# Performance work log

Hardware: AMD Instinct MI355X
Metric: run time of the kernel (lower is better)

The kernel has to match this reference:

```python
import jax, jax.numpy as jnp
import numpy as np

DIM = 64
B, H, W = 4, 80, 80


def setup_inputs() -> dict:
    key = jax.random.key(0)
    k1, k2, k3 = jax.random.split(key, 3)
    x = jax.random.normal(k1, (B, DIM, H, W), dtype=jnp.float32)
    # 1x1 conv == per-pixel linear: weight [3*dim, dim], bias [3*dim]
    w_qkv = jax.random.normal(k2, (3 * DIM, DIM), dtype=jnp.float32) * (1.0 / np.sqrt(DIM).astype(np.float32))
    b_qkv = jax.random.normal(k3, (3 * DIM,), dtype=jnp.float32) * 0.01
    return {"x": x, "w_qkv": w_qkv, "b_qkv": b_qkv}


def reference(x, w_qkv, b_qkv):
    Bb, C, Hh, Ww = x.shape
    N = Hh * Ww
    # 1x1 conv -> qkv, chunked along channels
    qkv = jnp.einsum('bchw,oc->bohw', x, w_qkv) + b_qkv[None, :, None, None]
    q, k, v = jnp.split(qkv, 3, axis=1)  # each [B,C,H,W]

    # --- spatial attention (uses q on both sides, as in the original) ---
    # qk: transpose(3,1) -> [B,W,H,C] -> [B, W*H, C]
    qk = jnp.transpose(q, (0, 3, 2, 1)).reshape(Bb, N, C)
    # kq: [B, C, H*W]  (note: different flatten order than qk, faithful to source)
    kq = q.reshape(Bb, C, N)
    ms = jax.nn.softmax(jnp.matmul(qk, kq), axis=-1)  # [B, N, N]

    # --- channel attention ---
    kf = k.reshape(Bb, C, N)                                # [B, C, N]
    qf = jnp.transpose(q, (0, 3, 2, 1)).reshape(Bb, N, C)   # [B, N, C]
    ma = jax.nn.softmax(jnp.matmul(kf, qf), axis=-1)        # [B, C, C]

    # --- apply to v ---
    vq = jnp.transpose(v, (0, 3, 2, 1)).reshape(Bb, N, C)   # [B, N, C]
    ms_out = jnp.matmul(ms, vq)                             # [B, N, C]
    ms_out = jnp.swapaxes(ms_out, 1, 2).reshape(Bb, C, Hh, Ww)
    ma_out = jnp.matmul(ma, v.reshape(Bb, C, N)).reshape(Bb, C, Hh, Ww)
    return ms_out + ma_out
```

## Files before the change

### kernel.cpp

```cpp
#include <hip/hip_runtime.h>
#include <stdint.h>

#define BATCH 4
#define CH 64
#define HW 80
#define NPIX 6400
#define SPLITS 3

typedef __attribute__((ext_vector_type(8))) short bf16x8;
typedef __attribute__((ext_vector_type(4))) float f32x4;

#define QSCALE 1.2011224087864498f
#define ESHIFT 115.41560327111707f

static __device__ __forceinline__ unsigned short f2bf(float f) {
  union { float f; unsigned int u; } v; v.f = f;
  unsigned int u = v.u;
  return (unsigned short)((u + 0x7fffu + ((u >> 16) & 1u)) >> 16);
}
static __device__ __forceinline__ float bf2f(unsigned short h) {
  union { unsigned int u; float f; } v; v.u = ((unsigned int)h) << 16;
  return v.f;
}
static __device__ __forceinline__ unsigned int split_pack(float a) {
  unsigned short hi = f2bf(a);
  union { unsigned int u; float f; } hf; hf.u = ((unsigned int)hi) << 16;
  unsigned short lo = f2bf(a - hf.f);
  return (unsigned int)hi | ((unsigned int)lo << 16);
}
static __device__ __forceinline__ void deint(uint4 a, uint4 b, bf16x8* h, bf16x8* l) {
  union { unsigned int u[4]; bf16x8 v; } H, L;
  H.u[0] = __builtin_amdgcn_perm(a.y, a.x, 0x05040100u);
  H.u[1] = __builtin_amdgcn_perm(a.w, a.z, 0x05040100u);
  H.u[2] = __builtin_amdgcn_perm(b.y, b.x, 0x05040100u);
  H.u[3] = __builtin_amdgcn_perm(b.w, b.z, 0x05040100u);
  L.u[0] = __builtin_amdgcn_perm(a.y, a.x, 0x07060302u);
  L.u[1] = __builtin_amdgcn_perm(a.w, a.z, 0x07060302u);
  L.u[2] = __builtin_amdgcn_perm(b.y, b.x, 0x07060302u);
  L.u[3] = __builtin_amdgcn_perm(b.w, b.z, 0x07060302u);
  *h = H.v; *l = L.v;
}

__global__ __launch_bounds__(512) void qkv_kernel(
    const float* __restrict__ x, const float* __restrict__ w,
    const float* __restrict__ bias, unsigned short* __restrict__ Qtbf,
    unsigned short* __restrict__ Vbf, unsigned int* __restrict__ Kpk,
    unsigned int* __restrict__ Qtn) {
  __shared__ float qs[64][65];
  int bid = blockIdx.x;
  int b = bid / 100, tile = bid % 100;
  int p0 = tile * 64;
  int t = threadIdx.x;
  int i = t & 63;
  int og = __builtin_amdgcn_readfirstlane(t >> 6);
  int p = p0 + i;
  int tp = (p % HW) * HW + p / HW;
  const float* xb = x + (size_t)b * CH * NPIX + p;
  float xv[64];
#pragma unroll
  for (int c = 0; c < 64; ++c) xv[c] = xb[(size_t)c * NPIX];
  size_t bc = (size_t)b * CH * NPIX;
  for (int j = 0; j < 24; j += 4) {
    int o = og * 24 + j;
    const float* wr0 = w + o * 64;
    const float* wr1 = wr0 + 64;
    const float* wr2 = wr0 + 128;
    const float* wr3 = wr0 + 192;
    float a0 = bias[o], a1 = bias[o + 1], a2 = bias[o + 2], a3 = bias[o + 3];
#pragma unroll
    for (int c = 0; c < 64; ++c) {
      float xc = xv[c];
      a0 += wr0[c] * xc;
      a1 += wr1[c] * xc;
      a2 += wr2[c] * xc;
      a3 += wr3[c] * xc;
    }
    float av[4] = {a0, a1, a2, a3};
#pragma unroll
    for (int u = 0; u < 4; ++u) {
      int oo = o + u;
      int cc = oo & 63;
      int kind = oo >> 6;
      float a = av[u];
      if (kind == 0) {
        qs[cc][i] = a;
        Qtn[bc + (size_t)cc * NPIX + tp] = split_pack(a);
      } else if (kind == 1) {
        Kpk[bc + (size_t)cc * NPIX + p] = split_pack(a);
      } else {
        Vbf[bc + (size_t)cc * NPIX + p] = f2bf(a);
      }
    }
  }
  __syncthreads();
  int j2 = t >> 3, g = t & 7;
  int pj = p0 + j2;
  int tpj = (pj % HW) * HW + pj / HW;
  unsigned int pk4[4];
#pragma unroll
  for (int q4 = 0; q4 < 4; ++q4) {
    float a0 = qs[g * 8 + q4 * 2][j2] * QSCALE;
    float a1 = qs[g * 8 + q4 * 2 + 1][j2] * QSCALE;
    pk4[q4] = (unsigned int)f2bf(a0) | ((unsigned int)f2bf(a1) << 16);
  }
  unsigned short* dst = Qtbf + ((size_t)b * NPIX + tpj) * 64 + g * 8;
  uint4 w0 = {pk4[0], pk4[1], pk4[2], pk4[3]};
  *(uint4*)&dst[0] = w0;
}

__global__ __launch_bounds__(256) void gram_kernel(
    const unsigned int* __restrict__ Kpk, const unsigned int* __restrict__ Qtn,
    float* __restrict__ Pc) {
  int bid = blockIdx.x;
  int b = bid / 100, chunk = bid % 100;
  int n0 = chunk * 64;
  int t = threadIdx.x;
  int w = t >> 6, lane = t & 63;
  int quad = lane >> 4, l16 = lane & 15;
  size_t bc = (size_t)b * CH * NPIX;

  f32x4 acc[4];
#pragma unroll
  for (int ct = 0; ct < 4; ++ct) acc[ct] = (f32x4){0.f, 0.f, 0.f, 0.f};

  const unsigned int* kp = Kpk + bc + (size_t)(w * 16 + l16) * NPIX + n0;
  bf16x8 ah[2], al[2];
#pragma unroll
  for (int ks2 = 0; ks2 < 2; ++ks2) {
    uint4 ua = *(const uint4*)&kp[ks2 * 32 + quad * 8];
    uint4 ub = *(const uint4*)&kp[ks2 * 32 + quad * 8 + 4];
    deint(ua, ub, &ah[ks2], &al[ks2]);
  }
#pragma unroll
  for (int ct = 0; ct < 4; ++ct) {
    const unsigned int* qp = Qtn + bc + (size_t)(ct * 16 + l16) * NPIX + n0;
#pragma unroll
    for (int ks2 = 0; ks2 < 2; ++ks2) {
      uint4 va = *(const uint4*)&qp[ks2 * 32 + quad * 8];
      uint4 vb = *(const uint4*)&qp[ks2 * 32 + quad * 8 + 4];
      bf16x8 bh, bl;
      deint(va, vb, &bh, &bl);
      acc[ct] = __builtin_amdgcn_mfma_f32_16x16x32_bf16(ah[ks2], bh, acc[ct], 0, 0, 0);
      acc[ct] = __builtin_amdgcn_mfma_f32_16x16x32_bf16(ah[ks2], bl, acc[ct], 0, 0, 0);
      acc[ct] = __builtin_amdgcn_mfma_f32_16x16x32_bf16(al[ks2], bh, acc[ct], 0, 0, 0);
    }
  }
#pragma unroll
  for (int ct = 0; ct < 4; ++ct)
#pragma unroll
    for (int r = 0; r < 4; ++r)
      atomicAdd(&Pc[((size_t)b * 64 + w * 16 + quad * 4 + r) * 64 + ct * 16 + l16],
                acc[ct][r]);
}

__global__ __launch_bounds__(256) void flash_kernel(
    const unsigned short* __restrict__ Qtbf, const unsigned short* __restrict__ Vbf,
    float* __restrict__ Opart, float* __restrict__ Lpart) {
  __shared__ char smem[40960] __attribute__((aligned(128)));

  int bid = blockIdx.x;
  int b = bid / 300;
  int rem = bid % 300;
  int qt = rem / 3, split = rem % 3;
  int p0 = qt * 64;
  int t = threadIdx.x;
  int w = t >> 6, lane = t & 63;
  int quad = lane >> 4, l16 = lane & 15;
  int sw = l16 & 7;
  size_t bq = (size_t)b * NPIX;
  size_t bC = (size_t)b * CH * NPIX;

  bf16x8 aq[2];
#pragma unroll
  for (int ks = 0; ks < 2; ++ks)
    aq[ks] = *(const bf16x8*)&Qtbf[(bq + p0 + w * 16 + l16) * 64 + ks * 32 + quad * 8];

  f32x4 oacc[4];
#pragma unroll
  for (int ct = 0; ct < 4; ++ct) oacc[ct] = (f32x4){0.f, 0.f, 0.f, 0.f};
  float psum = 0.f;

  const unsigned short* Kb = Qtbf + bq * 64;
  const unsigned short* Vb = Vbf + bC;
  int r0 = t >> 3, s0 = t & 7;
  int r1 = r0 + 32;
  int wOff0 = r0 * 64 + ((s0 ^ (r0 & 7)) << 3);
  int wOff1 = r1 * 64 + ((s0 ^ (r1 & 7)) << 3);

  int kt0 = split * 34;
  int niter = (split == 2) ? 32 : 34;

  unsigned short* Pw = (unsigned short*)(smem + 32768) + w * 16 * 64;

  uint4 kreg0, kreg1, vreg0, vreg1;
  {
    int n0 = kt0 * 64;
    kreg0 = *(const uint4*)&Kb[(size_t)(n0 + r0) * 64 + s0 * 8];
    vreg0 = *(const uint4*)&Vb[(size_t)r0 * NPIX + n0 + s0 * 8];
    kreg1 = *(const uint4*)&Kb[(size_t)(n0 + r1) * 64 + s0 * 8];
    vreg1 = *(const uint4*)&Vb[(size_t)r1 * NPIX + n0 + s0 * 8];
  }
  {
    unsigned short* K0 = (unsigned short*)smem;
    unsigned short* V0 = (unsigned short*)(smem + 16384);
    *(uint4*)&K0[wOff0] = kreg0;
    *(uint4*)&V0[wOff0] = vreg0;
    *(uint4*)&K0[wOff1] = kreg1;
    *(uint4*)&V0[wOff1] = vreg1;
  }
  {
    int n1 = (kt0 + 1) * 64;
    kreg0 = *(const uint4*)&Kb[(size_t)(n1 + r0) * 64 + s0 * 8];
    vreg0 = *(const uint4*)&Vb[(size_t)r0 * NPIX + n1 + s0 * 8];
    kreg1 = *(const uint4*)&Kb[(size_t)(n1 + r1) * 64 + s0 * 8];
    vreg1 = *(const uint4*)&Vb[(size_t)r1 * NPIX + n1 + s0 * 8];
  }
  __syncthreads();

  for (int it = 0; it < niter; ++it) {
    int cur = it & 1;
    unsigned short* Ksc = (unsigned short*)(smem + (cur << 13));
    unsigned short* Vsc = (unsigned short*)(smem + 16384 + (cur << 13));
    if (it + 1 < niter) {
      unsigned short* Kn = (unsigned short*)(smem + ((cur ^ 1) << 13));
      unsigned short* Vn = (unsigned short*)(smem + 16384 + ((cur ^ 1) << 13));
      *(uint4*)&Kn[wOff0] = kreg0;
      *(uint4*)&Vn[wOff0] = vreg0;
      *(uint4*)&Kn[wOff1] = kreg1;
      *(uint4*)&Vn[wOff1] = vreg1;
    }
    if (it + 2 < niter) {
      int n2 = (kt0 + it + 2) * 64;
      kreg0 = *(const uint4*)&Kb[(size_t)(n2 + r0) * 64 + s0 * 8];
      vreg0 = *(const uint4*)&Vb[(size_t)r0 * NPIX + n2 + s0 * 8];
      kreg1 = *(const uint4*)&Kb[(size_t)(n2 + r1) * 64 + s0 * 8];
      vreg1 = *(const uint4*)&Vb[(size_t)r1 * NPIX + n2 + s0 * 8];
    }
    f32x4 sc[4];
#pragma unroll
    for (int ct = 0; ct < 4; ++ct)
      sc[ct] = (f32x4){-ESHIFT, -ESHIFT, -ESHIFT, -ESHIFT};
    __builtin_amdgcn_s_setprio(1);
#pragma unroll
    for (int ks = 0; ks < 2; ++ks)
#pragma unroll
      for (int ct = 0; ct < 4; ++ct) {
        bf16x8 bk = *(const bf16x8*)&Ksc[(ct * 16 + l16) * 64 +
                                         (((ks * 4 + quad) ^ sw) << 3)];
        sc[ct] = __builtin_amdgcn_mfma_f32_16x16x32_bf16(bk, aq[ks], sc[ct], 0, 0, 0);
      }
    __builtin_amdgcn_s_setprio(0);
#pragma unroll
    for (int ct = 0; ct < 4; ++ct) {
      float e0 = __builtin_amdgcn_exp2f(sc[ct][0]);
      float e1 = __builtin_amdgcn_exp2f(sc[ct][1]);
      float e2 = __builtin_amdgcn_exp2f(sc[ct][2]);
      float e3 = __builtin_amdgcn_exp2f(sc[ct][3]);
      psum += (e0 + e1) + (e2 + e3);
      unsigned int pk0, pk1;
      asm("v_cvt_pk_bf16_f32 %0, %1, %2" : "=v"(pk0) : "v"(e0), "v"(e1));
      asm("v_cvt_pk_bf16_f32 %0, %1, %2" : "=v"(pk1) : "v"(e2), "v"(e3));
      uint2 pk = {pk0, pk1};
      *(uint2*)&Pw[l16 * 64 +
                   (((2 * ct + (quad >> 1)) ^ sw) << 3) + ((quad & 1) << 2)] = pk;
    }
    bf16x8 pf[2];
#pragma unroll
    for (int ks = 0; ks < 2; ++ks)
      pf[ks] = *(const bf16x8*)&Pw[l16 * 64 + (((ks * 4 + quad) ^ sw) << 3)];
    __builtin_amdgcn_s_setprio(1);
#pragma unroll
    for (int ks = 0; ks < 2; ++ks)
#pragma unroll
      for (int ct = 0; ct < 4; ++ct) {
        bf16x8 vf = *(const bf16x8*)&Vsc[(ct * 16 + l16) * 64 +
                                         (((ks * 4 + quad) ^ sw) << 3)];
        oacc[ct] = __builtin_amdgcn_mfma_f32_16x16x32_bf16(vf, pf[ks], oacc[ct], 0, 0, 0);
      }
    __builtin_amdgcn_s_setprio(0);
    __syncthreads();
  }
  float* Op = Opart + (size_t)(split * BATCH + b) * CH * NPIX;
  int pcol = p0 + w * 16 + l16;
  {
    float s = psum;
    s += __shfl_xor(s, 16, 64);
    s += __shfl_xor(s, 32, 64);
    if (quad == 0) Lpart[(size_t)(split * BATCH + b) * NPIX + pcol] = s;
  }
#pragma unroll
  for (int ct = 0; ct < 4; ++ct)
#pragma unroll
    for (int r = 0; r < 4; ++r)
      Op[(size_t)(ct * 16 + quad * 4 + r) * NPIX + pcol] = oacc[ct][r];
}

__global__ __launch_bounds__(256) void finalize_kernel(
    const float* __restrict__ Pc, const unsigned short* __restrict__ Vbf,
    const float* __restrict__ Opart, const float* __restrict__ Lpart,
    float* __restrict__ out) {
  __shared__ float maT[64 * 64];
  int bid = blockIdx.x;
  int b = bid / 100, nt = bid % 100;
  int t = threadIdx.x;
  if (t < 64) {
    int c = t;
    const float* row = Pc + ((size_t)b * 64 + c) * 64;
    float v[64];
    float mx = -1e30f;
#pragma unroll
    for (int j = 0; j < 64; ++j) { v[j] = row[j]; mx = fmaxf(mx, v[j]); }
    float s = 0.f;
#pragma unroll
    for (int j = 0; j < 64; ++j) { v[j] = __expf(v[j] - mx); s += v[j]; }
    float inv = 1.f / s;
#pragma unroll
    for (int j = 0; j < 64; ++j) maT[j * 64 + c] = v[j] * inv;
  }
  __syncthreads();
  int lane = t & 63, ct = t >> 6;
  int n = nt * 64 + lane;
  size_t bc = (size_t)b * CH * NPIX;
  const unsigned short* vb = Vbf + bc + n;
  float acc[16];
#pragma unroll
  for (int j = 0; j < 16; ++j) acc[j] = 0.f;
  for (int cp = 0; cp < 64; ++cp) {
    float vv = bf2f(vb[(size_t)cp * NPIX]);
    const float* m = &maT[cp * 64 + ct * 16];
    f32x4 m0 = *(const f32x4*)&m[0];
    f32x4 m1 = *(const f32x4*)&m[4];
    f32x4 m2 = *(const f32x4*)&m[8];
    f32x4 m3 = *(const f32x4*)&m[12];
#pragma unroll
    for (int j = 0; j < 4; ++j) {
      acc[j] += m0[j] * vv;
      acc[4 + j] += m1[j] * vv;
      acc[8 + j] += m2[j] * vv;
      acc[12 + j] += m3[j] * vv;
    }
  }
  float lsum = Lpart[(size_t)(0 * BATCH + b) * NPIX + n] +
               Lpart[(size_t)(1 * BATCH + b) * NPIX + n] +
               Lpart[(size_t)(2 * BATCH + b) * NPIX + n];
  float inv = 1.f / lsum;
  const float* O0 = Opart + (size_t)(0 * BATCH + b) * CH * NPIX;
  const float* O1 = Opart + (size_t)(1 * BATCH + b) * CH * NPIX;
  const float* O2 = Opart + (size_t)(2 * BATCH + b) * CH * NPIX;
#pragma unroll
  for (int j = 0; j < 16; ++j) {
    size_t co = (size_t)(ct * 16 + j) * NPIX + n;
    float o = O0[co] + O1[co] + O2[co];
    out[bc + co] = acc[j] + o * inv;
  }
}

extern "C" void kernel_launch(void* const* d_in, const int* in_sizes, int n_in,
                              void* d_out, int out_size, void* d_ws, size_t ws_size,
                              hipStream_t stream) {
  const float* x = (const float*)d_in[0];
  const float* w = (const float*)d_in[1];
  const float* bias = (const float*)d_in[2];
  float* out = (float*)d_out;
  char* ws = (char*)d_ws;
  unsigned short* Qtbf = (unsigned short*)(ws);
  unsigned short* Vbf = (unsigned short*)(ws + 3276800);
  unsigned int* Kpk = (unsigned int*)(ws + 6553600);
  unsigned int* Qtn = (unsigned int*)(ws + 13107200);
  float* Opart = (float*)(ws + 6553600);
  float* Pc = (float*)(ws + 26214400);
  float* Lpart = (float*)(ws + 26279936);

  hipMemsetAsync(Pc, 0, 65536, stream);
  qkv_kernel<<<400, 512, 0, stream>>>(x, w, bias, Qtbf, Vbf, Kpk, Qtn);
  gram_kernel<<<400, 256, 0, stream>>>(Kpk, Qtn, Pc);
  flash_kernel<<<1200, 256, 0, stream>>>(Qtbf, Vbf, Opart, Lpart);
  finalize_kernel<<<400, 256, 0, stream>>>(Pc, Vbf, Opart, Lpart, out);
}
```

Before: 177.9 us.

## Software-pipeline PV matmul one tile behind QK and single-buffer K

Restructures the flash loop so the P·V MFMAs for the previous key tile run after the current tile's QK and exp, with P and V double-buffered in shared memory and K single-buffered. The global prefetch distance drops from two tiles to one, and an epilogue handles the last tile's PV. It also adds a launch-bounds occupancy hint of 4 blocks per CU. The aim is to overlap exp/softmax work with matrix-core work and to cut register and LDS pressure, at the cost of two barriers per iteration and less prefetch lead time.

```diff
diff --git a/kernel.cpp b/kernel.cpp
--- a/kernel.cpp
+++ b/kernel.cpp
@@ -153,7 +153,7 @@
                 acc[ct][r]);
 }
 
-__global__ __launch_bounds__(256) void flash_kernel(
+__global__ __launch_bounds__(256, 4) void flash_kernel(
     const unsigned short* __restrict__ Qtbf, const unsigned short* __restrict__ Vbf,
     float* __restrict__ Opart, float* __restrict__ Lpart) {
   __shared__ char smem[40960] __attribute__((aligned(128)));
@@ -190,7 +190,9 @@
   int kt0 = split * 34;
   int niter = (split == 2) ? 32 : 34;
 
-  unsigned short* Pw = (unsigned short*)(smem + 32768) + w * 16 * 64;
+  unsigned short* Ks = (unsigned short*)smem;
+  unsigned short* VsB = (unsigned short*)(smem + 8192);
+  unsigned short* PbB = (unsigned short*)(smem + 24576);
 
   uint4 kreg0, kreg1, vreg0, vreg1;
   {
@@ -199,42 +201,35 @@
     vreg0 = *(const uint4*)&Vb[(size_t)r0 * NPIX + n0 + s0 * 8];
     kreg1 = *(const uint4*)&Kb[(size_t)(n0 + r1) * 64 + s0 * 8];
     vreg1 = *(const uint4*)&Vb[(size_t)r1 * NPIX + n0 + s0 * 8];
-  }
-  {
-    unsigned short* K0 = (unsigned short*)smem;
-    unsigned short* V0 = (unsigned short*)(smem + 16384);
-    *(uint4*)&K0[wOff0] = kreg0;
-    *(uint4*)&V0[wOff0] = vreg0;
-    *(uint4*)&K0[wOff1] = kreg1;
-    *(uint4*)&V0[wOff1] = vreg1;
-  }
-  {
-    int n1 = (kt0 + 1) * 64;
-    kreg0 = *(const uint4*)&Kb[(size_t)(n1 + r0) * 64 + s0 * 8];
-    vreg0 = *(const uint4*)&Vb[(size_t)r0 * NPIX + n1 + s0 * 8];
-    kreg1 = *(const uint4*)&Kb[(size_t)(n1 + r1) * 64 + s0 * 8];
-    vreg1 = *(const uint4*)&Vb[(size_t)r1 * NPIX + n1 + s0 * 8];
+    *(uint4*)&Ks[wOff0] = kreg0;
+    *(uint4*)&Ks[wOff1] = kreg1;
+    *(uint4*)&VsB[wOff0] = vreg0;
+    *(uint4*)&VsB[wOff1] = vreg1;
   }
   __syncthreads();
 
   for (int it = 0; it < niter; ++it) {
-    int cur = it & 1;
-    unsigned short* Ksc = (unsigned short*)(smem + (cur << 13));
-    unsigned short* Vsc = (unsigned short*)(smem + 16384 + (cur << 13));
-    if (it + 1 < niter) {
-      unsigned short* Kn = (unsigned short*)(smem + ((cur ^ 1) << 13));
-      unsigned short* Vn = (unsigned short*)(smem + 16384 + ((cur ^ 1) << 13));
-      *(uint4*)&Kn[wOff0] = kreg0;
+    if (it > 0) {
+      __syncthreads();
+      unsigned short* Vn = VsB + ((it & 1) << 12);
+      *(uint4*)&Ks[wOff0] = kreg0;
+      *(uint4*)&Ks[wOff1] = kreg1;
       *(uint4*)&Vn[wOff0] = vreg0;
-      *(uint4*)&Kn[wOff1] = kreg1;
       *(uint4*)&Vn[wOff1] = vreg1;
-    }
-    if (it + 2 < niter) {
-      int n2 = (kt0 + it + 2) * 64;
-      kreg0 = *(const uint4*)&Kb[(size_t)(n2 + r0) * 64 + s0 * 8];
-      vreg0 = *(const uint4*)&Vb[(size_t)r0 * NPIX + n2 + s0 * 8];
-      kreg1 = *(const uint4*)&Kb[(size_t)(n2 + r1) * 64 + s0 * 8];
-      vreg1 = *(const uint4*)&Vb[(size_t)r1 * NPIX + n2 + s0 * 8];
+      __syncthreads();
+    }
+    bf16x8 pf[2], vf[8];
+    if (it > 0) {
+      unsigned short* Pprev = PbB + (((it - 1) & 1) << 12) + w * 1024;
+      pf[0] = *(const bf16x8*)&Pprev[l16 * 64 + (((0 * 4 + quad) ^ sw) << 3)];
+      pf[1] = *(const bf16x8*)&Pprev[l16 * 64 + (((1 * 4 + quad) ^ sw) << 3)];
+      unsigned short* Vprev = VsB + (((it - 1) & 1) << 12);
+#pragma unroll
+      for (int ks = 0; ks < 2; ++ks)
+#pragma unroll
+        for (int ct = 0; ct < 4; ++ct)
+          vf[ks * 4 + ct] = *(const bf16x8*)&Vprev[(ct * 16 + l16) * 64 +
+                                                   (((ks * 4 + quad) ^ sw) << 3)];
     }
     f32x4 sc[4];
 #pragma unroll
@@ -245,11 +240,19 @@
     for (int ks = 0; ks < 2; ++ks)
 #pragma unroll
       for (int ct = 0; ct < 4; ++ct) {
-        bf16x8 bk = *(const bf16x8*)&Ksc[(ct * 16 + l16) * 64 +
-                                         (((ks * 4 + quad) ^ sw) << 3)];
+        bf16x8 bk = *(const bf16x8*)&Ks[(ct * 16 + l16) * 64 +
+                                        (((ks * 4 + quad) ^ sw) << 3)];
         sc[ct] = __builtin_amdgcn_mfma_f32_16x16x32_bf16(bk, aq[ks], sc[ct], 0, 0, 0);
       }
     __builtin_amdgcn_s_setprio(0);
+    if (it + 1 < niter) {
+      int n1 = (kt0 + it + 1) * 64;
+      kreg0 = *(const uint4*)&Kb[(size_t)(n1 + r0) * 64 + s0 * 8];
+      vreg0 = *(const uint4*)&Vb[(size_t)r0 * NPIX + n1 + s0 * 8];
+      kreg1 = *(const uint4*)&Kb[(size_t)(n1 + r1) * 64 + s0 * 8];
+      vreg1 = *(const uint4*)&Vb[(size_t)r1 * NPIX + n1 + s0 * 8];
+    }
+    unsigned short* Pw = PbB + ((it & 1) << 12) + w * 1024;
 #pragma unroll
     for (int ct = 0; ct < 4; ++ct) {
       float e0 = __builtin_amdgcn_exp2f(sc[ct][0]);
@@ -264,21 +267,35 @@
       *(uint2*)&Pw[l16 * 64 +
                    (((2 * ct + (quad >> 1)) ^ sw) << 3) + ((quad & 1) << 2)] = pk;
     }
-    bf16x8 pf[2];
+    if (it > 0) {
+      __builtin_amdgcn_s_setprio(1);
+#pragma unroll
+      for (int ks = 0; ks < 2; ++ks)
+#pragma unroll
+        for (int ct = 0; ct < 4; ++ct)
+          oacc[ct] = __builtin_amdgcn_mfma_f32_16x16x32_bf16(vf[ks * 4 + ct], pf[ks],
+                                                             oacc[ct], 0, 0, 0);
+      __builtin_amdgcn_s_setprio(0);
+    }
+  }
+  {
+    bf16x8 pf[2], vf[8];
+    unsigned short* Pprev = PbB + (((niter - 1) & 1) << 12) + w * 1024;
+    pf[0] = *(const bf16x8*)&Pprev[l16 * 64 + (((0 * 4 + quad) ^ sw) << 3)];
+    pf[1] = *(const bf16x8*)&Pprev[l16 * 64 + (((1 * 4 + quad) ^ sw) << 3)];
+    unsigned short* Vprev = VsB + (((niter - 1) & 1) << 12);
 #pragma unroll
     for (int ks = 0; ks < 2; ++ks)
-      pf[ks] = *(const bf16x8*)&Pw[l16 * 64 + (((ks * 4 + quad) ^ sw) << 3)];
-    __builtin_amdgcn_s_setprio(1);
+#pragma unroll
+      for (int ct = 0; ct < 4; ++ct)
+        vf[ks * 4 + ct] = *(const bf16x8*)&Vprev[(ct * 16 + l16) * 64 +
+                                                 (((ks * 4 + quad) ^ sw) << 3)];
 #pragma unroll
     for (int ks = 0; ks < 2; ++ks)
 #pragma unroll
-      for (int ct = 0; ct < 4; ++ct) {
-        bf16x8 vf = *(const bf16x8*)&Vsc[(ct * 16 + l16) * 64 +
-                                         (((ks * 4 + quad) ^ sw) << 3)];
-        oacc[ct] = __builtin_amdgcn_mfma_f32_16x16x32_bf16(vf, pf[ks], oacc[ct], 0, 0, 0);
-      }
-    __builtin_amdgcn_s_setprio(0);
-    __syncthreads();
+      for (int ct = 0; ct < 4; ++ct)
+        oacc[ct] = __builtin_amdgcn_mfma_f32_16x16x32_bf16(vf[ks * 4 + ct], pf[ks],
+                                                           oacc[ct], 0, 0, 0);
   }
   float* Op = Opart + (size_t)(split * BATCH + b) * CH * NPIX;
   int pcol = p0 + w * 16 + l16;
```

Measured after the change: 175.3 us. About the same (-1.4%).
